# Kernel tuning notes

Measured on AMD Instinct MI355X. Metric: run time of the kernel, lower is better.

The kernel has to match this reference:

```python
import jax, jax.numpy as jnp
from jax import lax
import numpy as np

B, T, C, N = 64, 1024, 1, 128  # batch, max seq len, num_conjugates, num_tags


def setup_inputs() -> dict:
    key = jax.random.key(0)
    ks = jax.random.split(key, 6)
    emissions = jax.random.normal(ks[0], (B, T, C, N), dtype=jnp.float32)
    token_sizes = jax.random.randint(ks[1], (B,), T // 2, T + 1)  # ragged lengths in [512, 1024]
    targets = jax.random.randint(ks[2], (B, T), 0, N)
    transitions = jax.random.normal(ks[3], (1, C, N, N), dtype=jnp.float32) * 0.1
    head_transitions = jax.random.normal(ks[4], (1, C, N), dtype=jnp.float32) * 0.1
    last_transitions = jax.random.normal(ks[5], (1, C, N), dtype=jnp.float32) * 0.1
    return dict(emissions=emissions, token_sizes=token_sizes, targets=targets,
                transitions=transitions, head_transitions=head_transitions,
                last_transitions=last_transitions)


def _crf(emissions, token_sizes, targets, transitions, head_transitions, last_transitions):
    # emissions: [B, T, C, N] padded; token_sizes: [B]; targets: [B, T]
    Bq, Tq, Cq, Nq = emissions.shape
    trans = transitions[0]          # [C, N, N]
    head = head_transitions[0]      # [C, N]
    last = last_transitions[0]      # [C, N]

    # ---- log partition (Log semiring forward algorithm; same math as the
    # log-depth semiring tree reduction in crf_partition) ----
    alpha0 = head[None, :, :] + emissions[:, 0]            # [B, C, N]
    emits = jnp.moveaxis(emissions[:, 1:], 1, 0)           # [T-1, B, C, N]
    valid = jnp.arange(1, Tq)[:, None] < token_sizes[None, :]  # [T-1, B]

    def step(alpha, inp):
        emit_t, v = inp
        # alpha[b,c,i] + trans[c,i,j] -> logsumexp over i
        new = jax.nn.logsumexp(alpha[:, :, :, None] + trans[None], axis=2) + emit_t
        return jnp.where(v[:, None, None], new, alpha), None

    alphaT, _ = lax.scan(step, alpha0, (emits, valid))
    log_partitions = jax.nn.logsumexp(alphaT + last[None, :, :], axis=-1)  # [B, C]

    # ---- path score (crf_segment_reduce with Log semiring) ----
    emit_sel = jnp.take_along_axis(emissions, targets[:, :, None, None], axis=3)[..., 0]  # [B, T, C]
    mask = (jnp.arange(Tq)[None, :] < token_sizes[:, None]).astype(emissions.dtype)       # [B, T]
    emit_sum = jnp.sum(emit_sel * mask[:, :, None], axis=1)                               # [B, C]

    prev_t, curr_t = targets[:, :-1], targets[:, 1:]
    trans_sel = trans[:, prev_t, curr_t]                                                  # [C, B, T-1]
    mask2 = (jnp.arange(1, Tq)[None, :] < token_sizes[:, None]).astype(emissions.dtype)   # [B, T-1]
    trans_sum = jnp.sum(trans_sel * mask2[None], axis=-1)                                 # [C, B]

    head_sel = head[:, targets[:, 0]]                                                     # [C, B]
    last_tag = jnp.take_along_axis(targets, (token_sizes - 1)[:, None], axis=1)[:, 0]     # [B]
    last_sel = last[:, last_tag]                                                          # [C, B]

    log_scores = emit_sum + trans_sum.T + head_sel.T + last_sel.T                         # [B, C]
    return jnp.stack([log_partitions, log_scores])  # [2, B, C]


def reference(emissions, token_sizes, targets, transitions, head_transitions, last_transitions):
    return _crf(emissions, token_sizes, targets, transitions, head_transitions, last_transitions)
```

## Files before the change

kernel.cpp:

```cpp
#include <hip/hip_runtime.h>
#include <math.h>

#define Bq 64
#define Tq 1024
#define Nq 128
#define SEG 129
#define NFW (SEG - 1)
#define NBW (SEG - 1)
#define WPC 16
#define LN2 0.6931471805599453f

typedef __attribute__((ext_vector_type(8))) _Float16 half8;
typedef __attribute__((ext_vector_type(2))) _Float16 h2;
typedef __attribute__((ext_vector_type(4))) float f32x4;

union BU { int u[4]; int4 v; half8 h; };
union E8 { int2 v; h2 p[2]; };
union E16 { int2 v2[2]; half8 h; };

__device__ __forceinline__ int pk16(float a, float b) {
    auto p = __builtin_amdgcn_cvt_pkrtz(a, b);
    return *(int*)&p;
}

__device__ __forceinline__ int MMAP(int q, int g, int j) {
    return 16 * (2 * q + (j >> 2)) + 4 * g + (j & 3);
}

__global__ __launch_bounds__(256)
void crf_prep_kernel(const float* __restrict__ em,
                     const float* __restrict__ trans,
                     const int* __restrict__ token_sizes,
                     const int* __restrict__ targets,
                     const float* __restrict__ head,
                     const float* __restrict__ last,
                     _Float16* __restrict__ eeh,
                     int4* __restrict__ aF, int4* __restrict__ aB,
                     float* __restrict__ out) {
    const int bid = blockIdx.x;
    const int tid = threadIdx.x;
    if (bid < 4096) {
        const int b = bid >> 6;
        const int row0 = (bid & 63) * 16;
        if (row0 >= token_sizes[b]) return;
        const size_t i = ((size_t)bid * 256 + tid) * 8;
        const float4* src = (const float4*)(em + i);
        float4 x0 = src[0], x1 = src[1];
        BU r;
        r.u[0] = pk16(__expf(x0.x), __expf(x0.y));
        r.u[1] = pk16(__expf(x0.z), __expf(x0.w));
        r.u[2] = pk16(__expf(x1.x), __expf(x1.y));
        r.u[3] = pk16(__expf(x1.z), __expf(x1.w));
        *(int4*)(eeh + i) = r.v;
        return;
    }
    if (bid < 4112) {
        const int fb = bid - 4096;
        const bool fwd = (fb < 8);
        const int kf = (fb & 7) * 4 + (tid >> 6);
        const int L = tid & 63;
        const int c = L & 15, g = L >> 4;
        const int r = kf >> 2, q = kf & 3;
        BU v;
        #pragma unroll
        for (int j = 0; j < 8; ++j) {
            const int m = MMAP(q, g, j);
            const int n = 16 * r + c;
            const float tv = fwd ? trans[m * Nq + n] : trans[n * Nq + m];
            v.h[j] = (_Float16)__expf(tv);
        }
        (fwd ? aF : aB)[kf * 64 + L] = v.v;
        return;
    }
    {
        const int b = bid - 4112;
        const int tsz = token_sizes[b];
        const int* tg = targets + b * Tq;
        const float* emc = em + (size_t)b * Tq * Nq;
        float sc = 0.f;
        for (int t = tid; t < tsz; t += 256) {
            int cur = tg[t];
            sc += emc[(size_t)t * Nq + cur];
            if (t >= 1) sc += trans[tg[t - 1] * Nq + cur];
        }
        #pragma unroll
        for (int off = 32; off >= 1; off >>= 1)
            sc += __shfl_xor(sc, off, 64);
        __shared__ float wsum[4];
        if ((tid & 63) == 0) wsum[tid >> 6] = sc;
        __syncthreads();
        if (tid == 0) {
            float tot = (wsum[0] + wsum[1]) + (wsum[2] + wsum[3]);
            out[Bq + b] = tot + head[tg[0]] + last[tg[tsz - 1]];
        }
    }
}

__device__ __forceinline__ void fwd_step(
    int k, int lenc, int lo, int hi, int g,
    const _Float16* __restrict__ eeh_c,
    const half8 (&afrag)[32], BU (&bf)[4],
    E8 (&eeCur)[8], E8 (&eeNxt)[8], int& Ecum)
{
    f32x4 acc[8];
    #pragma unroll
    for (int r = 0; r < 8; ++r) {
        f32x4 z = {0.f, 0.f, 0.f, 0.f};
        z = __builtin_amdgcn_mfma_f32_16x16x32_f16(afrag[r*4+0], bf[0].h, z, 0, 0, 0);
        z = __builtin_amdgcn_mfma_f32_16x16x32_f16(afrag[r*4+1], bf[1].h, z, 0, 0, 0);
        z = __builtin_amdgcn_mfma_f32_16x16x32_f16(afrag[r*4+2], bf[2].h, z, 0, 0, 0);
        z = __builtin_amdgcn_mfma_f32_16x16x32_f16(afrag[r*4+3], bf[3].h, z, 0, 0, 0);
        acc[r] = z;
    }
    {
        const int tn = min(lo + k, hi);
        const _Float16* bp = eeh_c + (size_t)tn * Nq;
        #pragma unroll
        for (int r = 0; r < 8; ++r)
            eeNxt[r].v = *(const int2*)(bp + 16*r + 4*g);
    }
    float w[32];
    float mx = 0.f;
    #pragma unroll
    for (int r = 0; r < 8; ++r) {
        #pragma unroll
        for (int i = 0; i < 4; ++i) {
            const float ee = (float)eeCur[r].p[i >> 1][i & 1];
            const float wv = acc[r][i] * ee;
            w[r*4+i] = wv;
            mx = fmaxf(mx, wv);
        }
    }
    mx = fmaxf(mx, __shfl_xor(mx, 16, 64));
    mx = fmaxf(mx, __shfl_xor(mx, 32, 64));
    const int eb = (__float_as_int(mx) >> 23) & 255;
    const float sig = __int_as_float((253 - eb) << 23);
    const bool act = (k <= lenc);
    #pragma unroll
    for (int q = 0; q < 4; ++q) {
        const int n0 = pk16(w[8*q+0]*sig, w[8*q+1]*sig);
        const int n1 = pk16(w[8*q+2]*sig, w[8*q+3]*sig);
        const int n2 = pk16(w[8*q+4]*sig, w[8*q+5]*sig);
        const int n3 = pk16(w[8*q+6]*sig, w[8*q+7]*sig);
        bf[q].u[0] = act ? n0 : bf[q].u[0];
        bf[q].u[1] = act ? n1 : bf[q].u[1];
        bf[q].u[2] = act ? n2 : bf[q].u[2];
        bf[q].u[3] = act ? n3 : bf[q].u[3];
    }
    Ecum += act ? (eb - 126) : 0;
}

__device__ __forceinline__ void bwd_step(
    int k, int lenc, int lo, int hi, int g,
    const _Float16* __restrict__ eeh_c,
    const half8 (&afrag)[32], BU (&bf)[4],
    E16 (&eeCur)[4], E16 (&eeNxt)[4], int& Ecum)
{
    BU beff[4];
    #pragma unroll
    for (int q = 0; q < 4; ++q) beff[q].h = bf[q].h * eeCur[q].h;
    f32x4 acc[8];
    #pragma unroll
    for (int r = 0; r < 8; ++r) {
        f32x4 z = {0.f, 0.f, 0.f, 0.f};
        z = __builtin_amdgcn_mfma_f32_16x16x32_f16(afrag[r*4+0], beff[0].h, z, 0, 0, 0);
        z = __builtin_amdgcn_mfma_f32_16x16x32_f16(afrag[r*4+1], beff[1].h, z, 0, 0, 0);
        z = __builtin_amdgcn_mfma_f32_16x16x32_f16(afrag[r*4+2], beff[2].h, z, 0, 0, 0);
        z = __builtin_amdgcn_mfma_f32_16x16x32_f16(afrag[r*4+3], beff[3].h, z, 0, 0, 0);
        acc[r] = z;
    }
    {
        const int tn = max(hi - k, lo);
        const _Float16* bp = eeh_c + (size_t)tn * Nq;
        #pragma unroll
        for (int q = 0; q < 4; ++q) {
            eeNxt[q].v2[0] = *(const int2*)(bp + 32*q + 4*g);
            eeNxt[q].v2[1] = *(const int2*)(bp + 32*q + 16 + 4*g);
        }
    }
    float mx = 0.f;
    #pragma unroll
    for (int r = 0; r < 8; ++r) {
        #pragma unroll
        for (int i = 0; i < 4; ++i) mx = fmaxf(mx, acc[r][i]);
    }
    mx = fmaxf(mx, __shfl_xor(mx, 16, 64));
    mx = fmaxf(mx, __shfl_xor(mx, 32, 64));
    const int eb = (__float_as_int(mx) >> 23) & 255;
    const float sig = __int_as_float((253 - eb) << 23);
    const bool act = (k <= lenc);
    #pragma unroll
    for (int q = 0; q < 4; ++q) {
        const int n0 = pk16(acc[2*q][0]*sig,   acc[2*q][1]*sig);
        const int n1 = pk16(acc[2*q][2]*sig,   acc[2*q][3]*sig);
        const int n2 = pk16(acc[2*q+1][0]*sig, acc[2*q+1][1]*sig);
        const int n3 = pk16(acc[2*q+1][2]*sig, acc[2*q+1][3]*sig);
        bf[q].u[0] = act ? n0 : bf[q].u[0];
        bf[q].u[1] = act ? n1 : bf[q].u[1];
        bf[q].u[2] = act ? n2 : bf[q].u[2];
        bf[q].u[3] = act ? n3 : bf[q].u[3];
    }
    Ecum += act ? (eb - 126) : 0;
}

__global__ __launch_bounds__(64, 1)
void crf_worker_kernel(const float* __restrict__ emissions,
                       const _Float16* __restrict__ eeh,
                       const int4* __restrict__ aF,
                       const int4* __restrict__ aB,
                       const int* __restrict__ token_sizes,
                       const float* __restrict__ head,
                       const float* __restrict__ last,
                       float* __restrict__ wsA, float* __restrict__ wsB,
                       float* __restrict__ wsLa, float* __restrict__ wsLb) {
    const int L = threadIdx.x;
    const int bid = blockIdx.x;

    const int b = bid >> 4;
    const int wv = bid & 15;
    const bool isFwd = (wv < 8);
    const int half_ = wv & 7;
    const int c = L & 15;
    const int g = L >> 4;
    const int s = (isFwd ? 1 : 2) + 16 * half_ + c;

    const float* em_c = emissions + (size_t)b * Tq * Nq;
    const _Float16* eeh_c = eeh + (size_t)b * Tq * Nq;
    const int tsz = token_sizes[b];
    const int nst = tsz - 1;
    const int base = nst / SEG;
    const int rem = nst % SEG;
    const int lo = 1 + (s - 1) * base + min(s - 1, rem);
    const int lenc = base + ((s <= rem) ? 1 : 0);
    const int hi = lo + lenc - 1;
    const int kmax = base + 1;

    half8 afrag[32];
    {
        const int4* asrc = isFwd ? aF : aB;
        #pragma unroll
        for (int kf = 0; kf < 32; ++kf) {
            BU t; t.v = asrc[kf * 64 + L];
            afrag[kf] = t.h;
        }
    }

    BU bf[4];
    float M0c;
    {
        float a0[32];
        float mx = -1e30f;
        #pragma unroll
        for (int q = 0; q < 4; ++q) {
            #pragma unroll
            for (int j2 = 0; j2 < 8; ++j2) {
                const int m = MMAP(q, g, j2);
                float v;
                if (isFwd) v = (s == 1)   ? (head[m] + em_c[m]) : 0.f;
                else       v = (s == SEG) ? last[m]             : 0.f;
                a0[q*8+j2] = v;
                mx = fmaxf(mx, v);
            }
        }
        mx = fmaxf(mx, __shfl_xor(mx, 16, 64));
        mx = fmaxf(mx, __shfl_xor(mx, 32, 64));
        M0c = mx;
        #pragma unroll
        for (int q = 0; q < 4; ++q) {
            #pragma unroll
            for (int p = 0; p < 4; ++p)
                bf[q].u[p] = pk16(__expf(a0[q*8+2*p]   - M0c),
                                  __expf(a0[q*8+2*p+1] - M0c));
        }
    }

    int Ecum = 0;
    int k = 1;
    if (isFwd) {
        E8 eeA[8], eeB8[8];
        const _Float16* bp = eeh_c + (size_t)lo * Nq;
        #pragma unroll
        for (int r = 0; r < 8; ++r) eeA[r].v = *(const int2*)(bp + 16*r + 4*g);
        for (; k + 1 <= kmax; k += 2) {
            fwd_step(k,   lenc, lo, hi, g, eeh_c, afrag, bf, eeA, eeB8, Ecum);
            fwd_step(k+1, lenc, lo, hi, g, eeh_c, afrag, bf, eeB8, eeA, Ecum);
        }
        if (k <= kmax)
            fwd_step(k, lenc, lo, hi, g, eeh_c, afrag, bf, eeA, eeB8, Ecum);
    } else {
        E16 eeA[4], eeB8[4];
        const _Float16* bp = eeh_c + (size_t)hi * Nq;
        #pragma unroll
        for (int q = 0; q < 4; ++q) {
            eeA[q].v2[0] = *(const int2*)(bp + 32*q + 4*g);
            eeA[q].v2[1] = *(const int2*)(bp + 32*q + 16 + 4*g);
        }
        for (; k + 1 <= kmax; k += 2) {
            bwd_step(k,   lenc, lo, hi, g, eeh_c, afrag, bf, eeA, eeB8, Ecum);
            bwd_step(k+1, lenc, lo, hi, g, eeh_c, afrag, bf, eeB8, eeA, Ecum);
        }
        if (k <= kmax)
            bwd_step(k, lenc, lo, hi, g, eeh_c, afrag, bf, eeA, eeB8, Ecum);
    }

    {
        float* dst = isFwd ? (wsA + ((size_t)(s - 1) * Bq + b) * Nq)
                           : (wsB + ((size_t)(s - 2) * Bq + b) * Nq);
        #pragma unroll
        for (int q = 0; q < 4; ++q) {
            f32x4 v0, v1;
            #pragma unroll
            for (int t = 0; t < 4; ++t) { v0[t] = (float)bf[q].h[t]; v1[t] = (float)bf[q].h[4+t]; }
            *(f32x4*)(dst + 32*q + 4*g)      = v0;
            *(f32x4*)(dst + 32*q + 16 + 4*g) = v1;
        }
        if (g == 0) {
            const float led = M0c + (float)Ecum * LN2;
            if (isFwd) wsLa[(s - 1) * Bq + b] = led;
            else       wsLb[(s - 2) * Bq + b] = led;
        }
    }
}

__global__ __launch_bounds__(1024)
void crf_combine_kernel(const float* __restrict__ wsA,
                        const float* __restrict__ wsB,
                        const float* __restrict__ wsLa,
                        const float* __restrict__ wsLb,
                        float* __restrict__ out) {
    const int chain = blockIdx.x;
    const int wq = threadIdx.x >> 6;
    const int l = threadIdx.x & 63;
    __shared__ float part[16];

    float tot = 0.f;
    #pragma unroll
    for (int rep = 0; rep < 8; ++rep) {
        const int j = wq + 16 * rep;
        const float* bb = wsB + ((size_t)j * Bq + chain) * Nq;
        const float* aa = wsA + ((size_t)j * Bq + chain) * Nq;
        float z = bb[l] * aa[l] + bb[l + 64] * aa[l + 64];
        float cc = bb[l] + bb[l + 64];
        #pragma unroll
        for (int off = 32; off >= 1; off >>= 1) {
            z  += __shfl_xor(z, off, 64);
            cc += __shfl_xor(cc, off, 64);
        }
        float term = __logf(z) + wsLa[j * Bq + chain];
        term += (j == NFW - 1) ? wsLb[(NBW - 1) * Bq + chain] : -__logf(cc);
        tot += term;
    }
    if (l == 0) part[wq] = tot;
    __syncthreads();
    if (threadIdx.x == 0) {
        float tz = 0.f;
        #pragma unroll
        for (int i = 0; i < 16; ++i) tz += part[i];
        out[chain] = tz;
    }
}

extern "C" void kernel_launch(void* const* d_in, const int* in_sizes, int n_in,
                              void* d_out, int out_size, void* d_ws, size_t ws_size,
                              hipStream_t stream) {
    const float* emissions   = (const float*)d_in[0];
    const int*   token_sizes = (const int*)d_in[1];
    const int*   targets     = (const int*)d_in[2];
    const float* transitions = (const float*)d_in[3];
    const float* head        = (const float*)d_in[4];
    const float* last        = (const float*)d_in[5];
    float* out = (float*)d_out;

    char* wp = (char*)d_ws;
    _Float16* eeh = (_Float16*)wp;                       wp += (size_t)Bq * Tq * Nq * 2;
    int4* aF = (int4*)wp;                                wp += 32 * 64 * 16;
    int4* aB = (int4*)wp;                                wp += 32 * 64 * 16;
    float* wsA  = (float*)wp;                            wp += (size_t)NFW * Bq * Nq * 4;
    float* wsB  = (float*)wp;                            wp += (size_t)NBW * Bq * Nq * 4;
    float* wsLa = (float*)wp;                            wp += NFW * Bq * 4;
    float* wsLb = (float*)wp;                            wp += NBW * Bq * 4;

    crf_prep_kernel<<<4096 + 16 + Bq, 256, 0, stream>>>(
        emissions, transitions, token_sizes, targets, head, last,
        eeh, aF, aB, out);
    crf_worker_kernel<<<Bq * WPC, 64, 0, stream>>>(
        emissions, eeh, aF, aB, token_sizes, head, last,
        wsA, wsB, wsLa, wsLb);
    crf_combine_kernel<<<Bq, 1024, 0, stream>>>(wsA, wsB, wsLa, wsLb, out);
}
```

Before: 38.59 us.

## Fuse emission exp into worker via LDS staging and move path score to combine

Drops the prep pass that wrote exp(emissions) as fp16 to global memory. Each worker now computes exp of its own short segment of emission rows, stages them in shared memory, and runs a fully unrolled sequence of at most 8 steps in one uniform form. The forward direction applies the emission factor as a B-operand multiply, with a final multiply by the hi row. The gold-path score computation moves into extra blocks of the combine kernel, so the prep kernel only builds the transition fragments. This removes a full-tensor write and read plus launch work, at the cost of redundant exp work inside the latency-bound worker.

```diff
diff --git a/kernel.cpp b/kernel.cpp
--- a/kernel.cpp
+++ b/kernel.cpp
@@ -15,8 +15,6 @@
 typedef __attribute__((ext_vector_type(4))) float f32x4;
 
 union BU { int u[4]; int4 v; half8 h; };
-union E8 { int2 v; h2 p[2]; };
-union E16 { int2 v2[2]; half8 h; };
 
 __device__ __forceinline__ int pk16(float a, float b) {
     auto p = __builtin_amdgcn_cvt_pkrtz(a, b);
@@ -27,138 +25,45 @@
     return 16 * (2 * q + (j >> 2)) + 4 * g + (j & 3);
 }
 
+__device__ __forceinline__ int4 packRowQ(const float* __restrict__ bp, int q, int g) {
+    const float4 x = *(const float4*)(bp + 32*q + 4*g);
+    const float4 y = *(const float4*)(bp + 32*q + 16 + 4*g);
+    return make_int4(pk16(__expf(x.x), __expf(x.y)),
+                     pk16(__expf(x.z), __expf(x.w)),
+                     pk16(__expf(y.x), __expf(y.y)),
+                     pk16(__expf(y.z), __expf(y.w)));
+}
+
 __global__ __launch_bounds__(256)
-void crf_prep_kernel(const float* __restrict__ em,
-                     const float* __restrict__ trans,
-                     const int* __restrict__ token_sizes,
-                     const int* __restrict__ targets,
-                     const float* __restrict__ head,
-                     const float* __restrict__ last,
-                     _Float16* __restrict__ eeh,
-                     int4* __restrict__ aF, int4* __restrict__ aB,
-                     float* __restrict__ out) {
-    const int bid = blockIdx.x;
-    const int tid = threadIdx.x;
-    if (bid < 4096) {
-        const int b = bid >> 6;
-        const int row0 = (bid & 63) * 16;
-        if (row0 >= token_sizes[b]) return;
-        const size_t i = ((size_t)bid * 256 + tid) * 8;
-        const float4* src = (const float4*)(em + i);
-        float4 x0 = src[0], x1 = src[1];
-        BU r;
-        r.u[0] = pk16(__expf(x0.x), __expf(x0.y));
-        r.u[1] = pk16(__expf(x0.z), __expf(x0.w));
-        r.u[2] = pk16(__expf(x1.x), __expf(x1.y));
-        r.u[3] = pk16(__expf(x1.z), __expf(x1.w));
-        *(int4*)(eeh + i) = r.v;
-        return;
-    }
-    if (bid < 4112) {
-        const int fb = bid - 4096;
-        const bool fwd = (fb < 8);
-        const int kf = (fb & 7) * 4 + (tid >> 6);
-        const int L = tid & 63;
-        const int c = L & 15, g = L >> 4;
-        const int r = kf >> 2, q = kf & 3;
-        BU v;
-        #pragma unroll
-        for (int j = 0; j < 8; ++j) {
-            const int m = MMAP(q, g, j);
-            const int n = 16 * r + c;
-            const float tv = fwd ? trans[m * Nq + n] : trans[n * Nq + m];
-            v.h[j] = (_Float16)__expf(tv);
-        }
-        (fwd ? aF : aB)[kf * 64 + L] = v.v;
-        return;
-    }
-    {
-        const int b = bid - 4112;
-        const int tsz = token_sizes[b];
-        const int* tg = targets + b * Tq;
-        const float* emc = em + (size_t)b * Tq * Nq;
-        float sc = 0.f;
-        for (int t = tid; t < tsz; t += 256) {
-            int cur = tg[t];
-            sc += emc[(size_t)t * Nq + cur];
-            if (t >= 1) sc += trans[tg[t - 1] * Nq + cur];
-        }
-        #pragma unroll
-        for (int off = 32; off >= 1; off >>= 1)
-            sc += __shfl_xor(sc, off, 64);
-        __shared__ float wsum[4];
-        if ((tid & 63) == 0) wsum[tid >> 6] = sc;
-        __syncthreads();
-        if (tid == 0) {
-            float tot = (wsum[0] + wsum[1]) + (wsum[2] + wsum[3]);
-            out[Bq + b] = tot + head[tg[0]] + last[tg[tsz - 1]];
-        }
-    }
-}
-
-__device__ __forceinline__ void fwd_step(
-    int k, int lenc, int lo, int hi, int g,
-    const _Float16* __restrict__ eeh_c,
-    const half8 (&afrag)[32], BU (&bf)[4],
-    E8 (&eeCur)[8], E8 (&eeNxt)[8], int& Ecum)
+void crf_prep_kernel(const float* __restrict__ trans,
+                     int4* __restrict__ aF, int4* __restrict__ aB) {
+    const int fb = blockIdx.x;
+    const bool fwd = (fb < 8);
+    const int kf = (fb & 7) * 4 + (threadIdx.x >> 6);
+    const int L = threadIdx.x & 63;
+    const int c = L & 15, g = L >> 4;
+    const int r = kf >> 2, q = kf & 3;
+    BU v;
+    #pragma unroll
+    for (int j = 0; j < 8; ++j) {
+        const int m = MMAP(q, g, j);
+        const int n = 16 * r + c;
+        const float tv = fwd ? trans[m * Nq + n] : trans[n * Nq + m];
+        v.h[j] = (_Float16)__expf(tv);
+    }
+    (fwd ? aF : aB)[kf * 64 + L] = v.v;
+}
+
+__device__ __forceinline__ void ustep(
+    int k, int lenc, int L,
+    const int4 (&eeL)[8][4][64],
+    const half8 (&afrag)[32], BU (&bf)[4], int& Ecum)
 {
-    f32x4 acc[8];
-    #pragma unroll
-    for (int r = 0; r < 8; ++r) {
-        f32x4 z = {0.f, 0.f, 0.f, 0.f};
-        z = __builtin_amdgcn_mfma_f32_16x16x32_f16(afrag[r*4+0], bf[0].h, z, 0, 0, 0);
-        z = __builtin_amdgcn_mfma_f32_16x16x32_f16(afrag[r*4+1], bf[1].h, z, 0, 0, 0);
-        z = __builtin_amdgcn_mfma_f32_16x16x32_f16(afrag[r*4+2], bf[2].h, z, 0, 0, 0);
-        z = __builtin_amdgcn_mfma_f32_16x16x32_f16(afrag[r*4+3], bf[3].h, z, 0, 0, 0);
-        acc[r] = z;
-    }
-    {
-        const int tn = min(lo + k, hi);
-        const _Float16* bp = eeh_c + (size_t)tn * Nq;
-        #pragma unroll
-        for (int r = 0; r < 8; ++r)
-            eeNxt[r].v = *(const int2*)(bp + 16*r + 4*g);
-    }
-    float w[32];
-    float mx = 0.f;
-    #pragma unroll
-    for (int r = 0; r < 8; ++r) {
-        #pragma unroll
-        for (int i = 0; i < 4; ++i) {
-            const float ee = (float)eeCur[r].p[i >> 1][i & 1];
-            const float wv = acc[r][i] * ee;
-            w[r*4+i] = wv;
-            mx = fmaxf(mx, wv);
-        }
-    }
-    mx = fmaxf(mx, __shfl_xor(mx, 16, 64));
-    mx = fmaxf(mx, __shfl_xor(mx, 32, 64));
-    const int eb = (__float_as_int(mx) >> 23) & 255;
-    const float sig = __int_as_float((253 - eb) << 23);
-    const bool act = (k <= lenc);
-    #pragma unroll
-    for (int q = 0; q < 4; ++q) {
-        const int n0 = pk16(w[8*q+0]*sig, w[8*q+1]*sig);
-        const int n1 = pk16(w[8*q+2]*sig, w[8*q+3]*sig);
-        const int n2 = pk16(w[8*q+4]*sig, w[8*q+5]*sig);
-        const int n3 = pk16(w[8*q+6]*sig, w[8*q+7]*sig);
-        bf[q].u[0] = act ? n0 : bf[q].u[0];
-        bf[q].u[1] = act ? n1 : bf[q].u[1];
-        bf[q].u[2] = act ? n2 : bf[q].u[2];
-        bf[q].u[3] = act ? n3 : bf[q].u[3];
-    }
-    Ecum += act ? (eb - 126) : 0;
-}
-
-__device__ __forceinline__ void bwd_step(
-    int k, int lenc, int lo, int hi, int g,
-    const _Float16* __restrict__ eeh_c,
-    const half8 (&afrag)[32], BU (&bf)[4],
-    E16 (&eeCur)[4], E16 (&eeNxt)[4], int& Ecum)
-{
-    BU beff[4];
-    #pragma unroll
-    for (int q = 0; q < 4; ++q) beff[q].h = bf[q].h * eeCur[q].h;
+    BU ee[4], beff[4];
+    #pragma unroll
+    for (int q = 0; q < 4; ++q) ee[q].v = eeL[k - 1][q][L];
+    #pragma unroll
+    for (int q = 0; q < 4; ++q) beff[q].h = bf[q].h * ee[q].h;
     f32x4 acc[8];
     #pragma unroll
     for (int r = 0; r < 8; ++r) {
@@ -168,15 +73,6 @@
         z = __builtin_amdgcn_mfma_f32_16x16x32_f16(afrag[r*4+2], beff[2].h, z, 0, 0, 0);
         z = __builtin_amdgcn_mfma_f32_16x16x32_f16(afrag[r*4+3], beff[3].h, z, 0, 0, 0);
         acc[r] = z;
-    }
-    {
-        const int tn = max(hi - k, lo);
-        const _Float16* bp = eeh_c + (size_t)tn * Nq;
-        #pragma unroll
-        for (int q = 0; q < 4; ++q) {
-            eeNxt[q].v2[0] = *(const int2*)(bp + 32*q + 4*g);
-            eeNxt[q].v2[1] = *(const int2*)(bp + 32*q + 16 + 4*g);
-        }
     }
     float mx = 0.f;
     #pragma unroll
@@ -205,7 +101,6 @@
 
 __global__ __launch_bounds__(64, 1)
 void crf_worker_kernel(const float* __restrict__ emissions,
-                       const _Float16* __restrict__ eeh,
                        const int4* __restrict__ aF,
                        const int4* __restrict__ aB,
                        const int* __restrict__ token_sizes,
@@ -216,6 +111,8 @@
     const int L = threadIdx.x;
     const int bid = blockIdx.x;
 
+    __shared__ __align__(16) int4 eeL[8][4][64];
+
     const int b = bid >> 4;
     const int wv = bid & 15;
     const bool isFwd = (wv < 8);
@@ -225,7 +122,6 @@
     const int s = (isFwd ? 1 : 2) + 16 * half_ + c;
 
     const float* em_c = emissions + (size_t)b * Tq * Nq;
-    const _Float16* eeh_c = eeh + (size_t)b * Tq * Nq;
     const int tsz = token_sizes[b];
     const int nst = tsz - 1;
     const int base = nst / SEG;
@@ -274,34 +170,42 @@
         }
     }
 
+    BU eeHi[4];
+    if (isFwd) {
+        const int one2 = pk16(1.0f, 1.0f);
+        const int4 ones = make_int4(one2, one2, one2, one2);
+        #pragma unroll
+        for (int q = 0; q < 4; ++q) eeL[0][q][L] = ones;
+        #pragma unroll
+        for (int i = 1; i < 8; ++i) {
+            const int row = min(lo + i - 1, hi - 1);
+            const float* bp = em_c + (size_t)row * Nq;
+            #pragma unroll
+            for (int q = 0; q < 4; ++q) eeL[i][q][L] = packRowQ(bp, q, g);
+        }
+        const float* bp = em_c + (size_t)hi * Nq;
+        #pragma unroll
+        for (int q = 0; q < 4; ++q) eeHi[q].v = packRowQ(bp, q, g);
+    } else {
+        #pragma unroll
+        for (int i = 0; i < 8; ++i) {
+            const int row = max(hi - i, lo);
+            const float* bp = em_c + (size_t)row * Nq;
+            #pragma unroll
+            for (int q = 0; q < 4; ++q) eeL[i][q][L] = packRowQ(bp, q, g);
+        }
+    }
+    __syncthreads();
+
     int Ecum = 0;
-    int k = 1;
-    if (isFwd) {
-        E8 eeA[8], eeB8[8];
-        const _Float16* bp = eeh_c + (size_t)lo * Nq;
-        #pragma unroll
-        for (int r = 0; r < 8; ++r) eeA[r].v = *(const int2*)(bp + 16*r + 4*g);
-        for (; k + 1 <= kmax; k += 2) {
-            fwd_step(k,   lenc, lo, hi, g, eeh_c, afrag, bf, eeA, eeB8, Ecum);
-            fwd_step(k+1, lenc, lo, hi, g, eeh_c, afrag, bf, eeB8, eeA, Ecum);
-        }
-        if (k <= kmax)
-            fwd_step(k, lenc, lo, hi, g, eeh_c, afrag, bf, eeA, eeB8, Ecum);
-    } else {
-        E16 eeA[4], eeB8[4];
-        const _Float16* bp = eeh_c + (size_t)hi * Nq;
-        #pragma unroll
-        for (int q = 0; q < 4; ++q) {
-            eeA[q].v2[0] = *(const int2*)(bp + 32*q + 4*g);
-            eeA[q].v2[1] = *(const int2*)(bp + 32*q + 16 + 4*g);
-        }
-        for (; k + 1 <= kmax; k += 2) {
-            bwd_step(k,   lenc, lo, hi, g, eeh_c, afrag, bf, eeA, eeB8, Ecum);
-            bwd_step(k+1, lenc, lo, hi, g, eeh_c, afrag, bf, eeB8, eeA, Ecum);
-        }
-        if (k <= kmax)
-            bwd_step(k, lenc, lo, hi, g, eeh_c, afrag, bf, eeA, eeB8, Ecum);
-    }
+    ustep(1, lenc, L, eeL, afrag, bf, Ecum);
+    ustep(2, lenc, L, eeL, afrag, bf, Ecum);
+    ustep(3, lenc, L, eeL, afrag, bf, Ecum);
+    ustep(4, lenc, L, eeL, afrag, bf, Ecum);
+    if (kmax >= 5) ustep(5, lenc, L, eeL, afrag, bf, Ecum);
+    if (kmax >= 6) ustep(6, lenc, L, eeL, afrag, bf, Ecum);
+    if (kmax >= 7) ustep(7, lenc, L, eeL, afrag, bf, Ecum);
+    if (kmax >= 8) ustep(8, lenc, L, eeL, afrag, bf, Ecum);
 
     {
         float* dst = isFwd ? (wsA + ((size_t)(s - 1) * Bq + b) * Nq)
@@ -310,7 +214,12 @@
         for (int q = 0; q < 4; ++q) {
             f32x4 v0, v1;
             #pragma unroll
-            for (int t = 0; t < 4; ++t) { v0[t] = (float)bf[q].h[t]; v1[t] = (float)bf[q].h[4+t]; }
+            for (int t = 0; t < 4; ++t) {
+                float m0 = isFwd ? (float)eeHi[q].h[t]     : 1.0f;
+                float m1 = isFwd ? (float)eeHi[q].h[4 + t] : 1.0f;
+                v0[t] = (float)bf[q].h[t]     * m0;
+                v1[t] = (float)bf[q].h[4 + t] * m1;
+            }
             *(f32x4*)(dst + 32*q + 4*g)      = v0;
             *(f32x4*)(dst + 32*q + 16 + 4*g) = v1;
         }
@@ -327,36 +236,70 @@
                         const float* __restrict__ wsB,
                         const float* __restrict__ wsLa,
                         const float* __restrict__ wsLb,
+                        const float* __restrict__ emissions,
+                        const int* __restrict__ token_sizes,
+                        const int* __restrict__ targets,
+                        const float* __restrict__ transitions,
+                        const float* __restrict__ head,
+                        const float* __restrict__ last,
                         float* __restrict__ out) {
-    const int chain = blockIdx.x;
-    const int wq = threadIdx.x >> 6;
-    const int l = threadIdx.x & 63;
+    const int bid = blockIdx.x;
+    const int tid = threadIdx.x;
     __shared__ float part[16];
 
-    float tot = 0.f;
-    #pragma unroll
-    for (int rep = 0; rep < 8; ++rep) {
-        const int j = wq + 16 * rep;
-        const float* bb = wsB + ((size_t)j * Bq + chain) * Nq;
-        const float* aa = wsA + ((size_t)j * Bq + chain) * Nq;
-        float z = bb[l] * aa[l] + bb[l + 64] * aa[l + 64];
-        float cc = bb[l] + bb[l + 64];
-        #pragma unroll
-        for (int off = 32; off >= 1; off >>= 1) {
-            z  += __shfl_xor(z, off, 64);
-            cc += __shfl_xor(cc, off, 64);
-        }
-        float term = __logf(z) + wsLa[j * Bq + chain];
-        term += (j == NFW - 1) ? wsLb[(NBW - 1) * Bq + chain] : -__logf(cc);
-        tot += term;
-    }
-    if (l == 0) part[wq] = tot;
-    __syncthreads();
-    if (threadIdx.x == 0) {
-        float tz = 0.f;
-        #pragma unroll
-        for (int i = 0; i < 16; ++i) tz += part[i];
-        out[chain] = tz;
+    if (bid < Bq) {
+        const int chain = bid;
+        const int wq = tid >> 6;
+        const int l = tid & 63;
+        float tot = 0.f;
+        #pragma unroll
+        for (int rep = 0; rep < 8; ++rep) {
+            const int j = wq + 16 * rep;
+            const float* bb = wsB + ((size_t)j * Bq + chain) * Nq;
+            const float* aa = wsA + ((size_t)j * Bq + chain) * Nq;
+            float z = bb[l] * aa[l] + bb[l + 64] * aa[l + 64];
+            float cc = bb[l] + bb[l + 64];
+            #pragma unroll
+            for (int off = 32; off >= 1; off >>= 1) {
+                z  += __shfl_xor(z, off, 64);
+                cc += __shfl_xor(cc, off, 64);
+            }
+            float term = __logf(z) + wsLa[j * Bq + chain];
+            term += (j == NFW - 1) ? wsLb[(NBW - 1) * Bq + chain] : -__logf(cc);
+            tot += term;
+        }
+        if (l == 0) part[wq] = tot;
+        __syncthreads();
+        if (tid == 0) {
+            float tz = 0.f;
+            #pragma unroll
+            for (int i = 0; i < 16; ++i) tz += part[i];
+            out[chain] = tz;
+        }
+        return;
+    }
+    {
+        const int b = bid - Bq;
+        const int tsz = token_sizes[b];
+        const int* tg = targets + b * Tq;
+        const float* emc = emissions + (size_t)b * Tq * Nq;
+        float sc = 0.f;
+        if (tid < tsz) {
+            const int cur = tg[tid];
+            sc = emc[(size_t)tid * Nq + cur];
+            if (tid >= 1) sc += transitions[tg[tid - 1] * Nq + cur];
+        }
+        #pragma unroll
+        for (int off = 32; off >= 1; off >>= 1)
+            sc += __shfl_xor(sc, off, 64);
+        if ((tid & 63) == 0) part[tid >> 6] = sc;
+        __syncthreads();
+        if (tid == 0) {
+            float tot = 0.f;
+            #pragma unroll
+            for (int i = 0; i < 16; ++i) tot += part[i];
+            out[Bq + b] = tot + head[tg[0]] + last[tg[tsz - 1]];
+        }
     }
 }
 
@@ -372,7 +315,6 @@
     float* out = (float*)d_out;
 
     char* wp = (char*)d_ws;
-    _Float16* eeh = (_Float16*)wp;                       wp += (size_t)Bq * Tq * Nq * 2;
     int4* aF = (int4*)wp;                                wp += 32 * 64 * 16;
     int4* aB = (int4*)wp;                                wp += 32 * 64 * 16;
     float* wsA  = (float*)wp;                            wp += (size_t)NFW * Bq * Nq * 4;
@@ -380,11 +322,11 @@
     float* wsLa = (float*)wp;                            wp += NFW * Bq * 4;
     float* wsLb = (float*)wp;                            wp += NBW * Bq * 4;
 
-    crf_prep_kernel<<<4096 + 16 + Bq, 256, 0, stream>>>(
-        emissions, transitions, token_sizes, targets, head, last,
-        eeh, aF, aB, out);
+    crf_prep_kernel<<<16, 256, 0, stream>>>(transitions, aF, aB);
     crf_worker_kernel<<<Bq * WPC, 64, 0, stream>>>(
-        emissions, eeh, aF, aB, token_sizes, head, last,
+        emissions, aF, aB, token_sizes, head, last,
         wsA, wsB, wsLa, wsLb);
-    crf_combine_kernel<<<Bq, 1024, 0, stream>>>(wsA, wsB, wsLa, wsLb, out);
-}
+    crf_combine_kernel<<<2 * Bq, 1024, 0, stream>>>(
+        wsA, wsB, wsLa, wsLb,
+        emissions, token_sizes, targets, transitions, head, last, out);
+}
```

New measurement: 36.92 us. 4.3% less time.
